# Optimization experiments

Measured on AMD Instinct MI355X. Metric: run time of the kernel, lower is better.

The kernel has to match this reference:

```python
import jax, jax.numpy as jnp
import numpy as np

N_SAMPLES = 2 ** 15  # 32768
NYQUIST = 22050.0 / 2.0
MIN_FREQ = 40.0 / NYQUIST
MAX_FREQ = 4000.0 / NYQUIST
FREQ_RANGE = MAX_FREQ - MIN_FREQ


def interp_linear(x, out_size):
    """torch F.interpolate(mode='linear', align_corners=False) along last axis."""
    in_size = x.shape[-1]
    scale = in_size / out_size
    coords = (jnp.arange(out_size, dtype=x.dtype) + 0.5) * scale - 0.5
    coords = jnp.clip(coords, 0.0, in_size - 1)
    lo = jnp.floor(coords).astype(jnp.int32)
    hi = jnp.minimum(lo + 1, in_size - 1)
    w = coords - lo.astype(x.dtype)
    return x[..., lo] * (1.0 - w) + x[..., hi] * w


def translate(pair, shift, scale):
    # angle of complex(pair[:,:,0], pair[:,:,1]) / pi, then affine
    angle = jnp.arctan2(pair[:, :, 1, :], pair[:, :, 0, :]) / np.pi
    return shift + angle * scale


def setup_inputs() -> dict:
    key = jax.random.key(0)
    k1, k2 = jax.random.split(key)
    x = jax.random.normal(k1, (16, 8, 10, 128), dtype=jnp.float32)
    noise = jax.random.normal(k2, (16, 8, N_SAMPLES), dtype=jnp.float32)
    return {"x": x, "noise": noise}


def reference(x, noise):
    # x: (batch, n_osc, 10, time_ctrl); noise: (batch, n_osc, N_SAMPLES)
    basic = x[:, :, 0:2, :]
    amp = jnp.sqrt(jnp.sum(basic * basic, axis=2))            # (b, o, t)
    amp = interp_linear(amp, N_SAMPLES)                       # (b, o, N)

    f0 = translate(basic, MIN_FREQ, FREQ_RANGE)               # control-rate
    mix = interp_linear(translate(x[:, :, 2:4, :], 1.0, 0.5), N_SAMPLES)
    harm_amp = amp * mix
    noise_amp = amp * (1.0 - mix)

    noise_std = translate(x[:, :, 4:6, :], MIN_FREQ, FREQ_RANGE)
    mod_factor = translate(x[:, :, 6:8, :], 0.25, 4.75)
    b = translate(x[:, :, 8:10, :], 0.1, 9.9)

    # band_filtered_noise: narrowband noise as a frequency-jittered sine
    f0_fr = interp_linear(f0, N_SAMPLES)
    std_fr = interp_linear(noise_std, N_SAMPLES)
    bfn = jnp.sin(jnp.cumsum(f0_fr + noise * std_fr, axis=-1))
    noise_sig = noise_amp * bfn

    mod_factor = interp_linear(mod_factor, N_SAMPLES)
    b = interp_linear(b, N_SAMPLES)
    mod = b * jnp.sin(jnp.cumsum(mod_factor, axis=-1))
    sig = harm_amp * jnp.sin(jnp.cumsum(f0_fr, axis=-1) + mod)

    mixed = noise_sig + sig                                   # (b, o, N)
    return jnp.mean(mixed, axis=1, keepdims=True)             # (b, 1, N)
```

## Files before the change

kernel.cpp:

```cpp
#include <hip/hip_runtime.h>
#include <math.h>

#define NS    32768
#define NB    128
#define NSEQ  128
#define CELL  16
#define NCELL (NS / CELL)
#define TPB1  1024
#define RUN   (NS / TPB1)
#define TPB2  256
#define GRID2 (16 * NCELL * 8 / TPB2)

__device__ __forceinline__ float sinr(float x) {
    return __builtin_amdgcn_sinf(x - rintf(x));
}

__device__ __forceinline__ void seg_params(int i, int& lo, int& hi,
                                           double& w0, double& wst) {
    if (i < 128)            { lo = 0;   hi = 1;   w0 = 0.0; wst = 0.0; }
    else if (i >= NS - 128) { lo = 127; hi = 127; w0 = 0.0; wst = 0.0; }
    else {
        lo = (i - 128) >> 8;  hi = lo + 1;
        int off = (i - 128) & 255;
        w0 = (off + 0.5) * (1.0 / 256.0);
        wst = 1.0 / 256.0;
    }
}

__global__ __launch_bounds__(TPB1)
void pre_kernel(const float* __restrict__ xg, const float* __restrict__ ng,
                double* __restrict__ wacc, float* __restrict__ wbins) {
    __shared__ double bf0[NB], bst[NB], bmf[NB];
    __shared__ double lred[TPB1 / 64][3];

    const double PI_    = 3.14159265358979323846;
    const double INV2PI = 0.15915494309189533576888376337251;
    const double MINF   = 40.0 / 11025.0;
    const double FRNG   = (4000.0 - 40.0) / 11025.0;

    int s    = blockIdx.x;
    int tid  = threadIdx.x;
    int lane = tid & 63;
    int wid  = tid >> 6;

    const float* xs = xg + s * 10 * NB;
    if (tid < 6 * NB) {
        int q = tid >> 7, j = tid & 127;
        double v;
        if (q == 0) {
            double a0 = (double)xs[j], a1 = (double)xs[NB + j];
            v = sqrt(a0 * a0 + a1 * a1);
        } else {
            int c2 = (q - 1) * 2;
            double ang = atan2((double)xs[(c2 + 1) * NB + j],
                               (double)xs[c2 * NB + j]) / PI_;
            double sh, sc;
            if      (q == 1) { sh = MINF; sc = FRNG; }
            else if (q == 2) { sh = 1.0;  sc = 0.5;  }
            else if (q == 3) { sh = MINF; sc = FRNG; }
            else if (q == 4) { sh = 0.25; sc = 4.75; }
            else             { sh = 0.1;  sc = 9.9;  }
            v = sh + ang * sc;
            if (q != 2) v *= INV2PI;
        }
        wbins[s * (6 * NB) + tid] = (float)v;
        if      (q == 1) bf0[j] = v;
        else if (q == 3) bst[j] = v;
        else if (q == 4) bmf[j] = v;
    }
    __syncthreads();

    int ci = tid * RUN;
    int lo, hi; double w0, wst;
    seg_params(ci, lo, hi, w0, wst);
    double f0L = bf0[lo], dF0 = bf0[hi] - f0L;
    double stL = bst[lo], dSt = bst[hi] - stL;
    double mfL = bmf[lo], dMf = bmf[hi] - mfL;

    const float4* nn4 = reinterpret_cast<const float4*>(ng + (size_t)s * NS + ci);
    double t1c[2], t3c[2], t2c[2];
    #pragma unroll
    for (int c = 0; c < 2; ++c) {
        double S0 = 0.0, S1 = 0.0;
        #pragma unroll
        for (int q4 = 0; q4 < 4; ++q4) {
            float4 nv = nn4[c * 4 + q4];
            double jd = (double)(q4 * 4);
            S0 += (double)nv.x; S1 += jd * (double)nv.x;
            S0 += (double)nv.y; S1 += (jd + 1.0) * (double)nv.y;
            S0 += (double)nv.z; S1 += (jd + 2.0) * (double)nv.z;
            S0 += (double)nv.w; S1 += (jd + 3.0) * (double)nv.w;
        }
        double wc = w0 + (double)(c * 16) * wst;
        double sw = 16.0 * wc + wst * 120.0;
        double t3 = 16.0 * f0L + dF0 * sw;
        double t2 = 16.0 * mfL + dMf * sw;
        double t1 = t3 + stL * S0 + dSt * (wc * S0 + wst * S1);
        t1c[c] = t1; t3c[c] = t3; t2c[c] = t2;
    }
    double r1 = t1c[0] + t1c[1], r3 = t3c[0] + t3c[1], r2 = t2c[0] + t2c[1];

    double v1 = r1, v3 = r3, v2 = r2;
    #pragma unroll
    for (int d = 1; d < 64; d <<= 1) {
        double u1 = __shfl_up(v1, d);
        double u3 = __shfl_up(v3, d);
        double u2 = __shfl_up(v2, d);
        if (lane >= d) { v1 += u1; v3 += u3; v2 += u2; }
    }
    if (lane == 63) { lred[wid][0] = v1; lred[wid][1] = v3; lred[wid][2] = v2; }
    __syncthreads();
    double b1 = 0.0, b3 = 0.0, b2 = 0.0;
    for (int k = 0; k < wid; ++k) {
        b1 += lred[k][0]; b3 += lred[k][1]; b2 += lred[k][2];
    }
    double e1 = b1 + v1 - r1, e3 = b3 + v3 - r3, e2 = b2 + v2 - r2;

    double* A = wacc + ((size_t)s * NCELL + (size_t)tid * 2) * 3;
    A[0] = e1;          A[1] = e3;          A[2] = e2;
    A[3] = e1 + t1c[0]; A[4] = e3 + t3c[0]; A[5] = e2 + t2c[0];
}

__global__ __launch_bounds__(TPB2)
void fm2_kernel(const float* __restrict__ ng, const double* __restrict__ wacc,
                const float* __restrict__ wbins, float* __restrict__ out) {
    int g  = blockIdx.x * TPB2 + threadIdx.x;
    int h  = g & 7;
    int q  = g >> 3;
    int b  = q >> 11;
    int c  = q & (NCELL - 1);
    int s  = (b << 3) + h;
    int i0 = c << 4;

    int lo, hi; double w0d, wstd;
    seg_params(i0, lo, hi, w0d, wstd);
    float w0  = (float)w0d;
    float wsf = (float)wstd;

    const float* B = wbins + s * (6 * NB);
    float amL = B[lo],          dAm = B[hi] - amL;
    float f0L = B[NB + lo],     dF0 = B[NB + hi] - f0L;
    float mxL = B[2 * NB + lo], dMx = B[2 * NB + hi] - mxL;
    float stL = B[3 * NB + lo], dSt = B[3 * NB + hi] - stL;
    float mfL = B[4 * NB + lo], dMf = B[4 * NB + hi] - mfL;
    float bbL = B[5 * NB + lo], dBb = B[5 * NB + hi] - bbL;

    const double* A = wacc + ((size_t)s * NCELL + c) * 3;
    double a1 = A[0], a3 = A[1], a2 = A[2];
    float fr1 = (float)(a1 - rint(a1));
    float fr3 = (float)(a3 - rint(a3));
    float fr2 = (float)(a2 - rint(a2));

    const float4* nn4 = reinterpret_cast<const float4*>(ng + (size_t)s * NS + i0);
    float4 nv0 = nn4[0], nv1 = nn4[1], nv2 = nn4[2], nv3 = nn4[3];
    float nf[CELL] = {nv0.x, nv0.y, nv0.z, nv0.w, nv1.x, nv1.y, nv1.z, nv1.w,
                      nv2.x, nv2.y, nv2.z, nv2.w, nv3.x, nv3.y, nv3.z, nv3.w};

    float arr[CELL];
    float d1 = 0.f, d2 = 0.f, d3 = 0.f;
    #pragma unroll
    for (int j = 0; j < CELL; ++j) {
        float wf  = fmaf((float)j, wsf, w0);
        float f0v = fmaf(wf, dF0, f0L);
        float stv = fmaf(wf, dSt, stL);
        float mfv = fmaf(wf, dMf, mfL);
        d3 += f0v;
        d1 += fmaf(nf[j], stv, f0v);
        d2 += mfv;
        float ampv = fmaf(wf, dAm, amL);
        float mixv = fmaf(wf, dMx, mxL);
        float bv   = fmaf(wf, dBb, bbL);
        float s2 = sinr(fr2 + d2);
        float s1 = sinr(fr1 + d1);
        float s3 = sinr(fmaf(bv, s2, fr3 + d3));
        float harm = ampv * mixv;
        arr[j] = fmaf(harm, s3, (ampv - harm) * s1);
    }

    #pragma unroll
    for (int m = 1; m <= 4; m <<= 1) {
        #pragma unroll
        for (int j = 0; j < CELL; ++j) arr[j] += __shfl_xor(arr[j], m);
    }
    if (h == 0) {
        float4* op = reinterpret_cast<float4*>(out + (size_t)b * NS + i0);
        #pragma unroll
        for (int j4 = 0; j4 < 4; ++j4)
            op[j4] = make_float4(arr[j4 * 4 + 0] * 0.125f, arr[j4 * 4 + 1] * 0.125f,
                                 arr[j4 * 4 + 2] * 0.125f, arr[j4 * 4 + 3] * 0.125f);
    }
}

extern "C" void kernel_launch(void* const* d_in, const int* in_sizes, int n_in,
                              void* d_out, int out_size, void* d_ws, size_t ws_size,
                              hipStream_t stream) {
    const float* x     = (const float*)d_in[0];
    const float* noise = (const float*)d_in[1];
    float* out = (float*)d_out;
    double* wacc = (double*)d_ws;
    float* wbins = (float*)(wacc + (size_t)NSEQ * NCELL * 3);
    pre_kernel<<<NSEQ, TPB1, 0, stream>>>(x, noise, wacc, wbins);
    fm2_kernel<<<GRID2, TPB2, 0, stream>>>(noise, wacc, wbins, out);
}
```

Measured before the change: 81.37 us.

## Restructure scan into per-part span totals plus fused local rescan

The first kernel, formerly 128 blocks each scanning one whole sequence, becomes 1024 small blocks that only emit per-512-sample part totals. The second kernel then rebuilds the prefix by summing the preceding part totals and rescans locally, and it computes the needed control bins itself instead of reading a per-cell prefix array. This spreads the first pass across many more CUs and shrinks the workspace traffic. In exchange the noise is read twice and atan2 bins are recomputed in both kernels.

```diff
diff --git a/kernel.cpp b/kernel.cpp
--- a/kernel.cpp
+++ b/kernel.cpp
@@ -1,15 +1,15 @@
 #include <hip/hip_runtime.h>
 #include <math.h>
 
-#define NS    32768
-#define NB    128
-#define NSEQ  128
-#define CELL  16
-#define NCELL (NS / CELL)
-#define TPB1  1024
-#define RUN   (NS / TPB1)
-#define TPB2  256
-#define GRID2 (16 * NCELL * 8 / TPB2)
+#define NS     32768
+#define NB     128
+#define CELL   16
+#define CPB    32
+#define PART   (CELL * CPB)
+#define NPARTS (NS / PART)
+#define TPB    256
+#define NBATCH 16
+#define GRID   (NBATCH * NPARTS)
 
 __device__ __forceinline__ float sinr(float x) {
     return __builtin_amdgcn_sinf(x - rintf(x));
@@ -27,143 +27,184 @@
     }
 }
 
-__global__ __launch_bounds__(TPB1)
-void pre_kernel(const float* __restrict__ xg, const float* __restrict__ ng,
-                double* __restrict__ wacc, float* __restrict__ wbins) {
-    __shared__ double bf0[NB], bst[NB], bmf[NB];
-    __shared__ double lred[TPB1 / 64][3];
-
+__device__ __forceinline__ double bin_value(const float* xs, int q, int j) {
     const double PI_    = 3.14159265358979323846;
     const double INV2PI = 0.15915494309189533576888376337251;
     const double MINF   = 40.0 / 11025.0;
     const double FRNG   = (4000.0 - 40.0) / 11025.0;
-
-    int s    = blockIdx.x;
-    int tid  = threadIdx.x;
-    int lane = tid & 63;
-    int wid  = tid >> 6;
-
-    const float* xs = xg + s * 10 * NB;
-    if (tid < 6 * NB) {
-        int q = tid >> 7, j = tid & 127;
-        double v;
-        if (q == 0) {
-            double a0 = (double)xs[j], a1 = (double)xs[NB + j];
-            v = sqrt(a0 * a0 + a1 * a1);
-        } else {
-            int c2 = (q - 1) * 2;
-            double ang = atan2((double)xs[(c2 + 1) * NB + j],
-                               (double)xs[c2 * NB + j]) / PI_;
-            double sh, sc;
-            if      (q == 1) { sh = MINF; sc = FRNG; }
-            else if (q == 2) { sh = 1.0;  sc = 0.5;  }
-            else if (q == 3) { sh = MINF; sc = FRNG; }
-            else if (q == 4) { sh = 0.25; sc = 4.75; }
-            else             { sh = 0.1;  sc = 9.9;  }
-            v = sh + ang * sc;
-            if (q != 2) v *= INV2PI;
-        }
-        wbins[s * (6 * NB) + tid] = (float)v;
-        if      (q == 1) bf0[j] = v;
-        else if (q == 3) bst[j] = v;
-        else if (q == 4) bmf[j] = v;
-    }
-    __syncthreads();
-
-    int ci = tid * RUN;
+    if (q == 0) {
+        double a0 = (double)xs[j], a1 = (double)xs[NB + j];
+        return sqrt(a0 * a0 + a1 * a1);
+    }
+    double ang = atan2((double)xs[(2 * q - 1) * NB + j],
+                       (double)xs[(2 * q - 2) * NB + j]) / PI_;
+    double sh, sc;
+    if      (q == 1) { sh = MINF; sc = FRNG; }
+    else if (q == 2) { sh = 1.0;  sc = 0.5;  }
+    else if (q == 3) { sh = MINF; sc = FRNG; }
+    else if (q == 4) { sh = 0.25; sc = 4.75; }
+    else             { sh = 0.1;  sc = 9.9;  }
+    double v = sh + ang * sc;
+    if (q != 2) v *= INV2PI;
+    return v;
+}
+
+__device__ __forceinline__ void cell_totals(
+        const float4* nn, double f0L, double dF0, double stL, double dSt,
+        double mfL, double dMf, double w0, double wst,
+        double& t1, double& t3, double& t2) {
+    float4 A0 = nn[0], A1 = nn[1], A2 = nn[2], A3 = nn[3];
+    float nf[CELL] = {A0.x, A0.y, A0.z, A0.w, A1.x, A1.y, A1.z, A1.w,
+                      A2.x, A2.y, A2.z, A2.w, A3.x, A3.y, A3.z, A3.w};
+    double S0 = 0.0, S1 = 0.0;
+    #pragma unroll
+    for (int j = 0; j < CELL; ++j) {
+        S0 += (double)nf[j];
+        S1 += (double)j * (double)nf[j];
+    }
+    double sw = 16.0 * w0 + 120.0 * wst;
+    t3 = 16.0 * f0L + dF0 * sw;
+    t2 = 16.0 * mfL + dMf * sw;
+    t1 = t3 + stL * S0 + dSt * (w0 * S0 + wst * S1);
+}
+
+__global__ __launch_bounds__(TPB, 4)
+void span_kernel(const float* __restrict__ xg, const float* __restrict__ ng,
+                 double* __restrict__ wspan) {
+    __shared__ double binsA[8][3][4];
+    __shared__ double wtot[4][8][3];
+
+    int bx = blockIdx.x, b = bx >> 6, p = bx & (NPARTS - 1);
+    int tid = threadIdx.x, lane = tid & 63, wid = tid >> 6;
+    int h = tid & 7, c = tid >> 3;
+    int P = p * PART;
+    int b0 = (P - 128) >> 8; if (b0 < 0) b0 = 0;
+
+    int s  = (b << 3) + h;
+    int i0 = P + c * CELL;
+    const float4* nn = reinterpret_cast<const float4*>(ng + (size_t)s * NS + i0);
+
+    if (tid < 96) {
+        int j = tid & 3, r = (tid >> 2) % 3, h2 = tid / 12;
+        int q = (r == 0) ? 1 : (r == 1) ? 3 : 4;
+        const float* xs = xg + (size_t)((b << 3) + h2) * 10 * NB;
+        binsA[h2][r][j] = bin_value(xs, q, min(b0 + j, NB - 1));
+    }
+    __syncthreads();
+
     int lo, hi; double w0, wst;
-    seg_params(ci, lo, hi, w0, wst);
-    double f0L = bf0[lo], dF0 = bf0[hi] - f0L;
-    double stL = bst[lo], dSt = bst[hi] - stL;
-    double mfL = bmf[lo], dMf = bmf[hi] - mfL;
-
-    const float4* nn4 = reinterpret_cast<const float4*>(ng + (size_t)s * NS + ci);
-    double t1c[2], t3c[2], t2c[2];
-    #pragma unroll
-    for (int c = 0; c < 2; ++c) {
-        double S0 = 0.0, S1 = 0.0;
-        #pragma unroll
-        for (int q4 = 0; q4 < 4; ++q4) {
-            float4 nv = nn4[c * 4 + q4];
-            double jd = (double)(q4 * 4);
-            S0 += (double)nv.x; S1 += jd * (double)nv.x;
-            S0 += (double)nv.y; S1 += (jd + 1.0) * (double)nv.y;
-            S0 += (double)nv.z; S1 += (jd + 2.0) * (double)nv.z;
-            S0 += (double)nv.w; S1 += (jd + 3.0) * (double)nv.w;
-        }
-        double wc = w0 + (double)(c * 16) * wst;
-        double sw = 16.0 * wc + wst * 120.0;
-        double t3 = 16.0 * f0L + dF0 * sw;
-        double t2 = 16.0 * mfL + dMf * sw;
-        double t1 = t3 + stL * S0 + dSt * (wc * S0 + wst * S1);
-        t1c[c] = t1; t3c[c] = t3; t2c[c] = t2;
-    }
-    double r1 = t1c[0] + t1c[1], r3 = t3c[0] + t3c[1], r2 = t2c[0] + t2c[1];
-
-    double v1 = r1, v3 = r3, v2 = r2;
-    #pragma unroll
-    for (int d = 1; d < 64; d <<= 1) {
+    seg_params(i0, lo, hi, w0, wst);
+    int jL = lo - b0, jH = hi - b0;
+    double f0L = binsA[h][0][jL], dF0 = binsA[h][0][jH] - f0L;
+    double stL = binsA[h][1][jL], dSt = binsA[h][1][jH] - stL;
+    double mfL = binsA[h][2][jL], dMf = binsA[h][2][jH] - mfL;
+
+    double t1, t3, t2;
+    cell_totals(nn, f0L, dF0, stL, dSt, mfL, dMf, w0, wst, t1, t3, t2);
+
+    double v1 = t1, v3 = t3, v2 = t2;
+    #pragma unroll
+    for (int d = 8; d < 64; d <<= 1) {
         double u1 = __shfl_up(v1, d);
         double u3 = __shfl_up(v3, d);
         double u2 = __shfl_up(v2, d);
         if (lane >= d) { v1 += u1; v3 += u3; v2 += u2; }
     }
-    if (lane == 63) { lred[wid][0] = v1; lred[wid][1] = v3; lred[wid][2] = v2; }
+    if (lane >= 56) { wtot[wid][h][0] = v1; wtot[wid][h][1] = v3; wtot[wid][h][2] = v2; }
+    __syncthreads();
+    if (tid < 24) {
+        int hh = tid & 7, k = tid >> 3;
+        double t = wtot[0][hh][k] + wtot[1][hh][k] + wtot[2][hh][k] + wtot[3][hh][k];
+        wspan[((size_t)(((b << 3) + hh) * NPARTS) + p) * 3 + k] = t;
+    }
+}
+
+__global__ __launch_bounds__(TPB, 4)
+void fm2_kernel(const float* __restrict__ xg, const float* __restrict__ ng,
+                const double* __restrict__ wspan, float* __restrict__ out) {
+    __shared__ double binsA[8][3][4];
+    __shared__ float  binsB[8][6][4];
+    __shared__ double wtot[4][8][3];
+    __shared__ double pref[8][3];
+
+    int bx = blockIdx.x, b = bx >> 6, p = bx & (NPARTS - 1);
+    int tid = threadIdx.x, lane = tid & 63, wid = tid >> 6;
+    int h = tid & 7, c = tid >> 3;
+    int P = p * PART;
+    int b0 = (P - 128) >> 8; if (b0 < 0) b0 = 0;
+
+    int s  = (b << 3) + h;
+    int i0 = P + c * CELL;
+    const float4* nn = reinterpret_cast<const float4*>(ng + (size_t)s * NS + i0);
+    float4 A0 = nn[0], A1 = nn[1], A2 = nn[2], A3 = nn[3];
+
+    if (tid < 192) {
+        int j = tid & 3, q = (tid >> 2) % 6, h2 = tid / 24;
+        const float* xs = xg + (size_t)((b << 3) + h2) * 10 * NB;
+        double v = bin_value(xs, q, min(b0 + j, NB - 1));
+        binsB[h2][q][j] = (float)v;
+        if      (q == 1) binsA[h2][0][j] = v;
+        else if (q == 3) binsA[h2][1][j] = v;
+        else if (q == 4) binsA[h2][2][j] = v;
+    } else if (tid < 216) {
+        int t2 = tid - 192, hh = t2 & 7, k = t2 >> 3;
+        const double* sp = wspan + ((size_t)(((b << 3) + hh) * NPARTS)) * 3 + k;
+        double acc = 0.0;
+        for (int q2 = 0; q2 < p; ++q2) acc += sp[q2 * 3];
+        pref[hh][k] = acc;
+    }
+    __syncthreads();
+
+    int lo, hi; double w0, wst;
+    seg_params(i0, lo, hi, w0, wst);
+    int jL = lo - b0, jH = hi - b0;
+    double f0L = binsA[h][0][jL], dF0 = binsA[h][0][jH] - f0L;
+    double stL = binsA[h][1][jL], dSt = binsA[h][1][jH] - stL;
+    double mfL = binsA[h][2][jL], dMf = binsA[h][2][jH] - mfL;
+
+    double t1, t3, t2;
+    cell_totals(nn, f0L, dF0, stL, dSt, mfL, dMf, w0, wst, t1, t3, t2);
+
+    double v1 = t1, v3 = t3, v2 = t2;
+    #pragma unroll
+    for (int d = 8; d < 64; d <<= 1) {
+        double u1 = __shfl_up(v1, d);
+        double u3 = __shfl_up(v3, d);
+        double u2 = __shfl_up(v2, d);
+        if (lane >= d) { v1 += u1; v3 += u3; v2 += u2; }
+    }
+    if (lane >= 56) { wtot[wid][h][0] = v1; wtot[wid][h][1] = v3; wtot[wid][h][2] = v2; }
     __syncthreads();
     double b1 = 0.0, b3 = 0.0, b2 = 0.0;
-    for (int k = 0; k < wid; ++k) {
-        b1 += lred[k][0]; b3 += lred[k][1]; b2 += lred[k][2];
-    }
-    double e1 = b1 + v1 - r1, e3 = b3 + v3 - r3, e2 = b2 + v2 - r2;
-
-    double* A = wacc + ((size_t)s * NCELL + (size_t)tid * 2) * 3;
-    A[0] = e1;          A[1] = e3;          A[2] = e2;
-    A[3] = e1 + t1c[0]; A[4] = e3 + t3c[0]; A[5] = e2 + t2c[0];
-}
-
-__global__ __launch_bounds__(TPB2)
-void fm2_kernel(const float* __restrict__ ng, const double* __restrict__ wacc,
-                const float* __restrict__ wbins, float* __restrict__ out) {
-    int g  = blockIdx.x * TPB2 + threadIdx.x;
-    int h  = g & 7;
-    int q  = g >> 3;
-    int b  = q >> 11;
-    int c  = q & (NCELL - 1);
-    int s  = (b << 3) + h;
-    int i0 = c << 4;
-
-    int lo, hi; double w0d, wstd;
-    seg_params(i0, lo, hi, w0d, wstd);
-    float w0  = (float)w0d;
-    float wsf = (float)wstd;
-
-    const float* B = wbins + s * (6 * NB);
-    float amL = B[lo],          dAm = B[hi] - amL;
-    float f0L = B[NB + lo],     dF0 = B[NB + hi] - f0L;
-    float mxL = B[2 * NB + lo], dMx = B[2 * NB + hi] - mxL;
-    float stL = B[3 * NB + lo], dSt = B[3 * NB + hi] - stL;
-    float mfL = B[4 * NB + lo], dMf = B[4 * NB + hi] - mfL;
-    float bbL = B[5 * NB + lo], dBb = B[5 * NB + hi] - bbL;
-
-    const double* A = wacc + ((size_t)s * NCELL + c) * 3;
-    double a1 = A[0], a3 = A[1], a2 = A[2];
+    #pragma unroll
+    for (int k = 0; k < 3; ++k)
+        if (wid > k) { b1 += wtot[k][h][0]; b3 += wtot[k][h][1]; b2 += wtot[k][h][2]; }
+
+    double a1 = pref[h][0] + b1 + (v1 - t1);
+    double a3 = pref[h][1] + b3 + (v3 - t3);
+    double a2 = pref[h][2] + b2 + (v2 - t2);
     float fr1 = (float)(a1 - rint(a1));
     float fr3 = (float)(a3 - rint(a3));
     float fr2 = (float)(a2 - rint(a2));
 
-    const float4* nn4 = reinterpret_cast<const float4*>(ng + (size_t)s * NS + i0);
-    float4 nv0 = nn4[0], nv1 = nn4[1], nv2 = nn4[2], nv3 = nn4[3];
-    float nf[CELL] = {nv0.x, nv0.y, nv0.z, nv0.w, nv1.x, nv1.y, nv1.z, nv1.w,
-                      nv2.x, nv2.y, nv2.z, nv2.w, nv3.x, nv3.y, nv3.z, nv3.w};
-
+    float amL = binsB[h][0][jL], dAm = binsB[h][0][jH] - amL;
+    float g0L = binsB[h][1][jL], gF0 = binsB[h][1][jH] - g0L;
+    float mxL = binsB[h][2][jL], dMx = binsB[h][2][jH] - mxL;
+    float gsL = binsB[h][3][jL], gSt = binsB[h][3][jH] - gsL;
+    float gmL = binsB[h][4][jL], gMf = binsB[h][4][jH] - gmL;
+    float bbL = binsB[h][5][jL], dBb = binsB[h][5][jH] - bbL;
+    float w0f = (float)w0, wsf = (float)wst;
+
+    float nf[CELL] = {A0.x, A0.y, A0.z, A0.w, A1.x, A1.y, A1.z, A1.w,
+                      A2.x, A2.y, A2.z, A2.w, A3.x, A3.y, A3.z, A3.w};
     float arr[CELL];
     float d1 = 0.f, d2 = 0.f, d3 = 0.f;
     #pragma unroll
     for (int j = 0; j < CELL; ++j) {
-        float wf  = fmaf((float)j, wsf, w0);
-        float f0v = fmaf(wf, dF0, f0L);
-        float stv = fmaf(wf, dSt, stL);
-        float mfv = fmaf(wf, dMf, mfL);
+        float wf  = fmaf((float)j, wsf, w0f);
+        float f0v = fmaf(wf, gF0, g0L);
+        float stv = fmaf(wf, gSt, gsL);
+        float mfv = fmaf(wf, gMf, gmL);
         d3 += f0v;
         d1 += fmaf(nf[j], stv, f0v);
         d2 += mfv;
@@ -197,8 +238,7 @@
     const float* x     = (const float*)d_in[0];
     const float* noise = (const float*)d_in[1];
     float* out = (float*)d_out;
-    double* wacc = (double*)d_ws;
-    float* wbins = (float*)(wacc + (size_t)NSEQ * NCELL * 3);
-    pre_kernel<<<NSEQ, TPB1, 0, stream>>>(x, noise, wacc, wbins);
-    fm2_kernel<<<GRID2, TPB2, 0, stream>>>(noise, wacc, wbins, out);
-}
+    double* wspan = (double*)d_ws;
+    span_kernel<<<GRID, TPB, 0, stream>>>(x, noise, wspan);
+    fm2_kernel<<<GRID, TPB, 0, stream>>>(x, noise, wspan, out);
+}
```

After: 85.42 us. 5.0% more time.
